# Kernel tuning notes

Measured on AMD Instinct MI355X. Metric: run time of the kernel, lower is better.

Reference implementation:

```python
import jax, jax.numpy as jnp
import numpy as np

HEADS = 12
DIM_HEAD = 64
SCALE = DIM_HEAD ** -0.5
LN_EPS = 1e-5


def _ternary(w):
    # BitNet-1.58-style ternary quantization with per-tensor absmean scale.
    s = jnp.mean(jnp.abs(w))
    return jnp.clip(jnp.round(w / (s + 1e-8)), -1.0, 1.0) * s


def _sparsify(x, sparsity):
    # Dynamic activation sparsity: zero the lowest-|x| `sparsity` fraction per token.
    thr = jnp.quantile(jnp.abs(x), sparsity, axis=-1, keepdims=True)
    return jnp.where(jnp.abs(x) >= thr, x, 0.0)


def setup_inputs() -> dict:
    key = jax.random.key(0)
    ks = jax.random.split(key, 4)
    b, n, dim = 16, 1024, 768
    inner = HEADS * DIM_HEAD
    return {
        "x": jax.random.normal(ks[0], (b, n, dim), dtype=jnp.float32),
        "gamma": jnp.ones((dim,), jnp.float32),
        "beta": jnp.zeros((dim,), jnp.float32),
        "w_qkv": jax.random.normal(ks[1], (3 * inner, dim), jnp.float32) * 0.02,
        "w_out": jax.random.normal(ks[2], (dim, inner), jnp.float32) * 0.02,
        "b_out": jnp.zeros((dim,), jnp.float32),
        "sparsity": jnp.float32(0.5),
    }


def reference(x, gamma, beta, w_qkv, w_out, b_out, sparsity):
    b, n, dim = x.shape
    # LayerNorm
    mu = jnp.mean(x, axis=-1, keepdims=True)
    var = jnp.mean((x - mu) ** 2, axis=-1, keepdims=True)
    xn = (x - mu) * jax.lax.rsqrt(var + LN_EPS) * gamma + beta
    # Sparse-ternary QKV projection (bias=False)
    qkv = jnp.einsum("bnd,ed->bne", _sparsify(xn, sparsity), _ternary(w_qkv))
    q, k, v = jnp.split(qkv, 3, axis=-1)
    def heads(t):  # b n (h d) -> b h n d
        return t.reshape(b, n, HEADS, DIM_HEAD).transpose(0, 2, 1, 3)
    q, k, v = heads(q), heads(k), heads(v)
    dots = jnp.einsum("bhid,bhjd->bhij", q, k) * SCALE
    attn = jax.nn.softmax(dots, axis=-1)
    out = jnp.einsum("bhij,bhjd->bhid", attn, v)
    out = out.transpose(0, 2, 1, 3).reshape(b, n, HEADS * DIM_HEAD)
    # Sparse-ternary output projection (with bias)
    out = jnp.einsum("bne,de->bnd", _sparsify(out, sparsity), _ternary(w_out)) + b_out
    return out
```

## Files before the change

kernel.cpp:

```cpp
#include <hip/hip_runtime.h>
#include <math.h>

#define TOKENS 16384
#define DIM    768
#define EDIM   2304
#define NHEADS 12
#define DHEAD  64
#define NQKVW  (EDIM*DIM)
#define NOUTW  (DIM*DIM)
#define LN_EPS 1e-5f

typedef __bf16 bf16x8 __attribute__((ext_vector_type(8)));
typedef float f32x4 __attribute__((ext_vector_type(4)));
typedef unsigned short u16x8 __attribute__((ext_vector_type(8)));
typedef unsigned short u16x4 __attribute__((ext_vector_type(4)));

__device__ __forceinline__ float wsum(float v){
#pragma unroll
  for(int m=1;m<64;m<<=1) v += __shfl_xor(v,m);
  return v;
}
__device__ __forceinline__ int wsumi(int v){
#pragma unroll
  for(int m=1;m<64;m<<=1) v += __shfl_xor(v,m);
  return v;
}
__device__ __forceinline__ unsigned wminu(unsigned v){
#pragma unroll
  for(int m=1;m<64;m<<=1){ unsigned o = __shfl_xor(v,m); v = (o<v)?o:v; }
  return v;
}

__device__ __forceinline__ unsigned short bf_rne(float x){
  unsigned u = __float_as_uint(x);
  unsigned r = (u + 0x7FFFu + ((u>>16)&1u)) >> 16;
  return (unsigned short)r;
}
__device__ __forceinline__ void split_bf(float x, unsigned short& h, unsigned short& l){
  h = bf_rne(x);
  float hf = __uint_as_float(((unsigned)h)<<16);
  l = bf_rne(x - hf);
}

__global__ __launch_bounds__(256) void absmean_kernel(
    const float* __restrict__ w1, int n1,
    const float* __restrict__ w2, int n2,
    double* __restrict__ sums){
  int stride = gridDim.x*blockDim.x;
  int i0 = blockIdx.x*blockDim.x + threadIdx.x;
  float s1=0.f, s2=0.f;
  for(int i=i0;i<n1;i+=stride) s1 += fabsf(w1[i]);
  for(int i=i0;i<n2;i+=stride) s2 += fabsf(w2[i]);
  double d1=(double)s1, d2=(double)s2;
#pragma unroll
  for(int m=1;m<64;m<<=1){ d1 += __shfl_xor(d1,m); d2 += __shfl_xor(d2,m); }
  __shared__ double l1[4], l2[4];
  int wv = threadIdx.x>>6;
  if((threadIdx.x&63)==0){ l1[wv]=d1; l2[wv]=d2; }
  __syncthreads();
  if(threadIdx.x==0){
    atomicAdd(&sums[0], l1[0]+l1[1]+l1[2]+l1[3]);
    atomicAdd(&sums[1], l2[0]+l2[1]+l2[2]+l2[3]);
  }
}

__global__ __launch_bounds__(256) void ternarize_kernel(
    const float* __restrict__ w, int n,
    const double* __restrict__ sums, int idx,
    unsigned short* __restrict__ o, float* __restrict__ scalef){
  float s  = (float)(sums[idx]/(double)n);
  float sd = s + 1e-8f;
  int i = blockIdx.x*blockDim.x + threadIdx.x;
  if(i<n){
    float t = rintf(w[i]/sd);
    t = fminf(fmaxf(t,-1.f),1.f);
    o[i] = bf_rne(t);
  }
  if(blockIdx.x==0 && threadIdx.x==0) scalef[idx] = s;
}

template<bool DO_LN>
__global__ __launch_bounds__(256) void ln_sparsify_kernel(
    const float* __restrict__ in,
    const float* __restrict__ gamma,
    const float* __restrict__ beta,
    const float* __restrict__ qp,
    unsigned short* __restrict__ oh,
    unsigned short* __restrict__ ol){
  int token = blockIdx.x*4 + (threadIdx.x>>6);
  int lane  = threadIdx.x & 63;
  const float* row = in + (size_t)token*DIM;
  float v[12];
#pragma unroll
  for(int g=0; g<3; ++g){
    float4 t = *(const float4*)(row + g*256 + lane*4);
    v[g*4+0]=t.x; v[g*4+1]=t.y; v[g*4+2]=t.z; v[g*4+3]=t.w;
  }
  float xn[12];
  if (DO_LN){
    float s=0.f;
#pragma unroll
    for(int i=0;i<12;i++) s += v[i];
    s = wsum(s);
    float mu = s*(1.f/768.f);
    float ss=0.f;
#pragma unroll
    for(int i=0;i<12;i++){ float d=v[i]-mu; ss += d*d; }
    ss = wsum(ss);
    float inv = 1.f/sqrtf(ss*(1.f/768.f) + LN_EPS);
#pragma unroll
    for(int g=0; g<3; ++g){
      float4 gm = *(const float4*)(gamma + g*256 + lane*4);
      float4 bt = *(const float4*)(beta  + g*256 + lane*4);
      xn[g*4+0] = (v[g*4+0]-mu)*inv*gm.x + bt.x;
      xn[g*4+1] = (v[g*4+1]-mu)*inv*gm.y + bt.y;
      xn[g*4+2] = (v[g*4+2]-mu)*inv*gm.z + bt.z;
      xn[g*4+3] = (v[g*4+3]-mu)*inv*gm.w + bt.w;
    }
  } else {
#pragma unroll
    for(int i=0;i<12;i++) xn[i]=v[i];
  }
  unsigned a[12];
#pragma unroll
  for(int i=0;i<12;i++) a[i] = __float_as_uint(fabsf(xn[i]));
  float q = *qp;
  float pos = q*767.f;
  int lo = (int)floorf(pos);
  lo = lo<0 ? 0 : (lo>767 ? 767 : lo);
  float frac = pos-(float)lo;
  unsigned prefix=0;
  int r = lo;
#pragma unroll 1
  for(int bit=30; bit>=0; --bit){
    unsigned cand = prefix | (1u<<bit);
    int c=0;
#pragma unroll
    for(int i=0;i<12;i++) c += (a[i]>=prefix && a[i]<cand) ? 1 : 0;
    c = wsumi(c);
    if(r>=c){ r-=c; prefix=cand; }
  }
  float f1 = __uint_as_float(prefix);
  float thr;
  if (frac>0.f && lo<767){
    int cle=0;
#pragma unroll
    for(int i=0;i<12;i++) cle += (a[i]<=prefix)?1:0;
    cle = wsumi(cle);
    unsigned mn=0xFFFFFFFFu;
#pragma unroll
    for(int i=0;i<12;i++){ if(a[i]>prefix && a[i]<mn) mn=a[i]; }
    mn = wminu(mn);
    float f2 = (cle>=lo+2) ? f1 : __uint_as_float(mn);
    thr = (frac>=0.5f) ? f2-(f2-f1)*(1.f-frac) : f1+(f2-f1)*frac;
  } else thr=f1;
  size_t obase = (size_t)token*DIM;
#pragma unroll
  for(int g=0; g<3; ++g){
    u16x4 hv, lv;
#pragma unroll
    for(int e=0;e<4;e++){
      float val = (fabsf(xn[g*4+e])>=thr) ? xn[g*4+e] : 0.f;
      unsigned short hh, ll;
      split_bf(val, hh, ll);
      hv[e]=hh; lv[e]=ll;
    }
    *(u16x4*)(oh + obase + g*256 + lane*4) = hv;
    *(u16x4*)(ol + obase + g*256 + lane*4) = lv;
  }
}

#define LDSW(row,c16) ((((row)*8 + ((c16) ^ ((row)&7))))*16)

template<int MODE>
__global__ __launch_bounds__(256) void gemm_sp_kernel(
    const unsigned short* __restrict__ ah, const unsigned short* __restrict__ al,
    const unsigned short* __restrict__ wt, const float* __restrict__ scalef,
    const float* __restrict__ bias,
    unsigned short* __restrict__ qh, unsigned short* __restrict__ ql,
    unsigned short* __restrict__ kh, unsigned short* __restrict__ kl,
    unsigned short* __restrict__ vth, unsigned short* __restrict__ vtl,
    float* __restrict__ outp){
  __shared__ __align__(16) char lds[49152];
  const int bm = blockIdx.y*128;
  const int bn = blockIdx.x*128;
  const int tid = threadIdx.x, w = tid>>6, l = tid&63, lq = l&15, g = l>>4;
  const int wm = (w>>1)*64, wn = (w&1)*64;

  const f32x4 zero4 = {0.f,0.f,0.f,0.f};
  f32x4 acc[4][4];
#pragma unroll
  for(int mt=0;mt<4;mt++)
#pragma unroll
    for(int nt=0;nt<4;nt++) acc[mt][nt]=zero4;

#pragma unroll 1
  for(int k0=0; k0<768; k0+=64){
    __syncthreads();
#pragma unroll
    for(int grp=0; grp<2; grp++){
      u16x8 tmp[6];
#pragma unroll
      for(int c=0;c<6;c++){
        int cc = grp*6 + c;
        int t = cc>>2;
        int slot = (cc&3)*256 + tid;
        int row = slot>>3, c8 = slot&7;
        int gc = ((c8 ^ (row&7)))<<3;
        const unsigned short* gp =
           (t==0) ? ah + (size_t)(bm+row)*768 + k0 + gc :
           (t==1) ? al + (size_t)(bm+row)*768 + k0 + gc :
                    wt + (size_t)(bn+row)*768 + k0 + gc;
        tmp[c] = *(const u16x8*)gp;
      }
#pragma unroll
      for(int c=0;c<6;c++){
        int cc = grp*6 + c;
        int t = cc>>2;
        int slot = (cc&3)*256 + tid;
        *(u16x8*)(lds + t*16384 + slot*16) = tmp[c];
      }
    }
    __syncthreads();
#pragma unroll
    for(int kc=0;kc<2;kc++){
      bf16x8 bfr[4];
#pragma unroll
      for(int nt=0;nt<4;nt++)
        bfr[nt] = *(const bf16x8*)(lds + 32768 + LDSW(wn+16*nt+lq, kc*4+g));
#pragma unroll
      for(int mt=0;mt<4;mt++){
        bf16x8 ahf = *(const bf16x8*)(lds +          LDSW(wm+16*mt+lq, kc*4+g));
        bf16x8 alf = *(const bf16x8*)(lds + 16384 +  LDSW(wm+16*mt+lq, kc*4+g));
#pragma unroll
        for(int nt=0;nt<4;nt++){
          acc[mt][nt] = __builtin_amdgcn_mfma_f32_16x16x32_bf16(ahf, bfr[nt], acc[mt][nt], 0,0,0);
          acc[mt][nt] = __builtin_amdgcn_mfma_f32_16x16x32_bf16(alf, bfr[nt], acc[mt][nt], 0,0,0);
        }
      }
    }
  }
  __syncthreads();

  if (MODE == 1){
    float s2 = scalef[1];
#pragma unroll
    for(int mt=0;mt<4;mt++)
#pragma unroll
      for(int nt=0;nt<4;nt++){
        int n = bn + wn + 16*nt + lq;
        float bs = bias[n];
#pragma unroll
        for(int r=0;r<4;r++){
          int m = bm + wm + 16*mt + 4*g + r;
          outp[(size_t)m*768 + n] = acc[mt][nt][r]*s2 + bs;
        }
      }
    return;
  }

  float s1 = scalef[0];
  if (bn < 1536){
    const bool isQ = bn < 768;
    const float sc = isQ ? s1*0.125f : s1;
    unsigned short* dh = isQ ? qh : kh;
    unsigned short* dl = isQ ? ql : kl;
    const int cb = isQ ? bn : bn-768;
    unsigned short* Th = (unsigned short*)lds;
    unsigned short* Tl = Th + 64*136;
#pragma unroll
    for(int p=0;p<2;p++){
      if(p) __syncthreads();
      if ((w>>1)==p){
#pragma unroll
        for(int mt=0;mt<4;mt++)
#pragma unroll
          for(int nt=0;nt<4;nt++)
#pragma unroll
            for(int r=0;r<4;r++){
              int mloc = 16*mt + 4*g + r;
              int c = wn + 16*nt + lq;
              unsigned short hh,ll;
              split_bf(acc[mt][nt][r]*sc, hh, ll);
              Th[mloc*136 + c] = hh;
              Tl[mloc*136 + c] = ll;
            }
      }
      __syncthreads();
      int mrow = tid>>2;
      int m = p*64 + mrow;
#pragma unroll
      for(int i=0;i<4;i++){
        int c8 = (tid&3)*4 + i;
        u16x8 hv = *(const u16x8*)(Th + mrow*136 + c8*8);
        u16x8 lv = *(const u16x8*)(Tl + mrow*136 + c8*8);
        size_t off = (size_t)(bm+m)*768 + cb + c8*8;
        *(u16x8*)(dh + off) = hv;
        *(u16x8*)(dl + off) = lv;
      }
    }
  } else {
    const int b  = bm >> 10;
    const int t0 = bm & 1023;
#pragma unroll
    for(int mt=0;mt<4;mt++)
#pragma unroll
      for(int nt=0;nt<4;nt++){
        int n = bn - 1536 + wn + 16*nt + lq;
        int hh_ = n>>6, d = n&63;
        u16x4 hv, lv;
#pragma unroll
        for(int r=0;r<4;r++){
          unsigned short h_, l_;
          split_bf(acc[mt][nt][r]*s1, h_, l_);
          hv[r]=h_; lv[r]=l_;
        }
        size_t off = ((size_t)(b*NHEADS + hh_)*64 + d)*1024 + t0 + wm + 16*mt + 4*g;
        *(u16x4*)(vth + off) = hv;
        *(u16x4*)(vtl + off) = lv;
      }
  }
}

__global__ __launch_bounds__(256) void attn_mfma_kernel(
    const unsigned short* __restrict__ qh, const unsigned short* __restrict__ ql,
    const unsigned short* __restrict__ kh, const unsigned short* __restrict__ kl,
    const unsigned short* __restrict__ vh, const unsigned short* __restrict__ vl,
    float* __restrict__ ao){
  __shared__ __align__(16) char lds[32768];
  const int qb=blockIdx.x, h=blockIdx.y, b=blockIdx.z;
  const int tid=threadIdx.x, w=tid>>6, l=tid&63, lq=l&15, g=l>>4;

  const int qtok = b*1024 + qb*64 + w*16 + lq;
  bf16x8 qhf[2], qlf[2];
  {
    const size_t qo = (size_t)qtok*768 + h*64 + g*8;
    qhf[0] = *(const bf16x8*)(qh + qo);
    qhf[1] = *(const bf16x8*)(qh + qo + 32);
    qlf[0] = *(const bf16x8*)(ql + qo);
    qlf[1] = *(const bf16x8*)(ql + qo + 32);
  }
  const f32x4 zero4 = {0.f,0.f,0.f,0.f};
  f32x4 o[4];
#pragma unroll
  for(int mt=0;mt<4;mt++) o[mt]=zero4;
  float ms = -INFINITY, ls = 0.f;

  for(int kt=0; kt<16; ++kt){
    __syncthreads();
#pragma unroll
    for(int m=0;m<4;m++){
      const unsigned short* src = (m==0)?kh:(m==1)?kl:(m==2)?vh:vl;
#pragma unroll
      for(int half=0; half<2; half++){
        int a = half*256 + tid;
        int row = a>>3;
        int c16 = (a&7)^(row&7);
        size_t goff = (m<2)
          ? ((size_t)(b*1024 + kt*64 + row)*768 + h*64 + c16*8)
          : (((size_t)(b*NHEADS + h)*64 + row)*1024 + kt*64 + c16*8);
        u16x8 v = *(const u16x8*)(src + goff);
        *(u16x8*)(lds + m*8192 + a*16) = v;
      }
    }
    __syncthreads();
    f32x4 s[4];
#pragma unroll
    for(int mt=0;mt<4;mt++) s[mt]=zero4;
#pragma unroll
    for(int kc=0;kc<2;kc++){
#pragma unroll
      for(int mt=0;mt<4;mt++){
        bf16x8 ka = *(const bf16x8*)(lds + 0*8192 + LDSW(16*mt+lq, 4*kc+g));
        bf16x8 kb = *(const bf16x8*)(lds + 1*8192 + LDSW(16*mt+lq, 4*kc+g));
        s[mt] = __builtin_amdgcn_mfma_f32_16x16x32_bf16(ka, qhf[kc], s[mt], 0,0,0);
        s[mt] = __builtin_amdgcn_mfma_f32_16x16x32_bf16(ka, qlf[kc], s[mt], 0,0,0);
        s[mt] = __builtin_amdgcn_mfma_f32_16x16x32_bf16(kb, qhf[kc], s[mt], 0,0,0);
      }
    }
    float pm = -INFINITY;
#pragma unroll
    for(int mt=0;mt<4;mt++)
#pragma unroll
      for(int r=0;r<4;r++) pm = fmaxf(pm, s[mt][r]);
    pm = fmaxf(pm, __shfl_xor(pm,16));
    pm = fmaxf(pm, __shfl_xor(pm,32));
    float mn = fmaxf(ms, pm);
    float alpha = __expf(ms - mn);
    float p[4][4];
    float rs = 0.f;
#pragma unroll
    for(int mt=0;mt<4;mt++)
#pragma unroll
      for(int r=0;r<4;r++){ float pv=__expf(s[mt][r]-mn); p[mt][r]=pv; rs+=pv; }
    rs += __shfl_xor(rs,16);
    rs += __shfl_xor(rs,32);
    ls = ls*alpha + rs; ms = mn;
#pragma unroll
    for(int mt=0;mt<4;mt++) o[mt] *= alpha;
    bf16x8 pfh[2], pfl[2];
#pragma unroll
    for(int c=0;c<2;c++){
      u16x8 hu, lu;
#pragma unroll
      for(int j=0;j<8;j++){
        int srcLane = lq + (((g&1)*2 + (j>>2))<<4);
        float va = __shfl(p[2*c  ][j&3], srcLane);
        float vb = __shfl(p[2*c+1][j&3], srcLane);
        float v = (g>>1) ? vb : va;
        unsigned short hh, ll;
        split_bf(v, hh, ll);
        hu[j]=hh; lu[j]=ll;
      }
      pfh[c] = __builtin_bit_cast(bf16x8, hu);
      pfl[c] = __builtin_bit_cast(bf16x8, lu);
    }
#pragma unroll
    for(int kc=0;kc<2;kc++){
#pragma unroll
      for(int mt=0;mt<4;mt++){
        bf16x8 va_ = *(const bf16x8*)(lds + 2*8192 + LDSW(16*mt+lq, 4*kc+g));
        bf16x8 vb_ = *(const bf16x8*)(lds + 3*8192 + LDSW(16*mt+lq, 4*kc+g));
        o[mt] = __builtin_amdgcn_mfma_f32_16x16x32_bf16(va_, pfh[kc], o[mt], 0,0,0);
        o[mt] = __builtin_amdgcn_mfma_f32_16x16x32_bf16(va_, pfl[kc], o[mt], 0,0,0);
        o[mt] = __builtin_amdgcn_mfma_f32_16x16x32_bf16(vb_, pfh[kc], o[mt], 0,0,0);
        o[mt] = __builtin_amdgcn_mfma_f32_16x16x32_bf16(vb_, pfl[kc], o[mt], 0,0,0);
      }
    }
  }
  float inv = 1.f/ls;
  float* orow = ao + (size_t)qtok*DIM + h*64;
#pragma unroll
  for(int mt=0;mt<4;mt++){
    f32x4 st = o[mt]*inv;
    *(f32x4*)(orow + mt*16 + g*4) = st;
  }
}

extern "C" void kernel_launch(void* const* d_in, const int* in_sizes, int n_in,
                              void* d_out, int out_size, void* d_ws, size_t ws_size,
                              hipStream_t stream){
  const float* x      = (const float*)d_in[0];
  const float* gamma  = (const float*)d_in[1];
  const float* beta   = (const float*)d_in[2];
  const float* w_qkv  = (const float*)d_in[3];
  const float* w_out  = (const float*)d_in[4];
  const float* b_out  = (const float*)d_in[5];
  const float* spars  = (const float*)d_in[6];
  float* out = (float*)d_out;

  double* sums  = (double*)d_ws;
  float* scalef = (float*)((char*)d_ws + 16);
  unsigned short* wt_qkv = (unsigned short*)((char*)d_ws + 64);
  unsigned short* wt_out = wt_qkv + NQKVW;
  unsigned short* ahb = wt_out + NOUTW;
  unsigned short* alb = ahb + (size_t)TOKENS*DIM;
  unsigned short* qh  = alb + (size_t)TOKENS*DIM;
  unsigned short* ql  = qh  + (size_t)TOKENS*DIM;
  unsigned short* kh  = ql  + (size_t)TOKENS*DIM;
  unsigned short* kl  = kh  + (size_t)TOKENS*DIM;
  unsigned short* vth = kl  + (size_t)TOKENS*DIM;
  unsigned short* vtl = vth + (size_t)TOKENS*DIM;
  float* ao = (float*)(vtl + (size_t)TOKENS*DIM);

  hipMemsetAsync(d_ws, 0, 16, stream);
  absmean_kernel<<<1024,256,0,stream>>>(w_qkv, NQKVW, w_out, NOUTW, sums);
  ternarize_kernel<<<(NQKVW+255)/256,256,0,stream>>>(w_qkv, NQKVW, sums, 0, wt_qkv, scalef);
  ternarize_kernel<<<(NOUTW+255)/256,256,0,stream>>>(w_out, NOUTW, sums, 1, wt_out, scalef);
  ln_sparsify_kernel<true><<<TOKENS/4,256,0,stream>>>(x, gamma, beta, spars, ahb, alb);
  gemm_sp_kernel<0><<<dim3(EDIM/128, TOKENS/128),256,0,stream>>>(
      ahb, alb, wt_qkv, scalef, nullptr, qh, ql, kh, kl, vth, vtl, nullptr);
  attn_mfma_kernel<<<dim3(16,NHEADS,16),256,0,stream>>>(qh, ql, kh, kl, vth, vtl, ao);
  ln_sparsify_kernel<false><<<TOKENS/4,256,0,stream>>>(ao, nullptr, nullptr, spars, ahb, alb);
  gemm_sp_kernel<1><<<dim3(DIM/128, TOKENS/128),256,0,stream>>>(
      ahb, alb, wt_out, scalef, b_out, nullptr, nullptr, nullptr, nullptr, nullptr, nullptr, out);
}
```

Measured before the change: 840.6 us.

## Add XCD-aware block remapping, larger attention blocks, and native bf16 conversions

The GEMM kernels now take a 1D grid and remap block ids so that consecutive tiles land on the same XCD, which should improve L2 reuse of A and weight tiles. The attention kernel moves to 512 threads covering 128 queries per block, also with XCD-grouped (batch, head) assignment, so each K/V tile loaded into LDS serves twice as many queries. Its LDS fill becomes one 16-byte load per tensor per thread. bf16 rounding now uses native __bf16 casts instead of manual bit arithmetic. The larger block may lower occupancy, and the remap assumes the hardware dispatches blocks round-robin across 8 XCDs.

```diff
diff --git a/kernel.cpp b/kernel.cpp
--- a/kernel.cpp
+++ b/kernel.cpp
@@ -31,15 +31,16 @@
   return v;
 }
 
+__device__ __forceinline__ void split_bf(float x, unsigned short& h, unsigned short& l){
+  __bf16 hb = (__bf16)x;
+  float hf = (float)hb;
+  __bf16 lb = (__bf16)(x - hf);
+  h = __builtin_bit_cast(unsigned short, hb);
+  l = __builtin_bit_cast(unsigned short, lb);
+}
 __device__ __forceinline__ unsigned short bf_rne(float x){
-  unsigned u = __float_as_uint(x);
-  unsigned r = (u + 0x7FFFu + ((u>>16)&1u)) >> 16;
-  return (unsigned short)r;
-}
-__device__ __forceinline__ void split_bf(float x, unsigned short& h, unsigned short& l){
-  h = bf_rne(x);
-  float hf = __uint_as_float(((unsigned)h)<<16);
-  l = bf_rne(x - hf);
+  __bf16 hb = (__bf16)x;
+  return __builtin_bit_cast(unsigned short, hb);
 }
 
 __global__ __launch_bounds__(256) void absmean_kernel(
@@ -182,8 +183,15 @@
     unsigned short* __restrict__ vth, unsigned short* __restrict__ vtl,
     float* __restrict__ outp){
   __shared__ __align__(16) char lds[49152];
-  const int bm = blockIdx.y*128;
-  const int bn = blockIdx.x*128;
+  const int NB = (MODE==0) ? 18 : 6;
+  const int nwg = NB*128;
+  int flat = blockIdx.x;
+  {
+    int xcd = flat & 7, idx = flat >> 3;
+    flat = xcd*(nwg>>3) + idx;
+  }
+  const int bm = (flat / NB)*128;
+  const int bn = (flat % NB)*128;
   const int tid = threadIdx.x, w = tid>>6, l = tid&63, lq = l&15, g = l>>4;
   const int wm = (w>>1)*64, wn = (w&1)*64;
 
@@ -322,16 +330,20 @@
   }
 }
 
-__global__ __launch_bounds__(256) void attn_mfma_kernel(
+__global__ __launch_bounds__(512) void attn_mfma_kernel(
     const unsigned short* __restrict__ qh, const unsigned short* __restrict__ ql,
     const unsigned short* __restrict__ kh, const unsigned short* __restrict__ kl,
     const unsigned short* __restrict__ vh, const unsigned short* __restrict__ vl,
     float* __restrict__ ao){
   __shared__ __align__(16) char lds[32768];
-  const int qb=blockIdx.x, h=blockIdx.y, b=blockIdx.z;
+  int flat = blockIdx.x;
+  int xcd = flat & 7, r_ = flat >> 3;
+  int pair = xcd*24 + (r_ >> 3);
+  int qb = r_ & 7;
+  int h = pair % NHEADS, b = pair / NHEADS;
   const int tid=threadIdx.x, w=tid>>6, l=tid&63, lq=l&15, g=l>>4;
 
-  const int qtok = b*1024 + qb*64 + w*16 + lq;
+  const int qtok = b*1024 + qb*128 + w*16 + lq;
   bf16x8 qhf[2], qlf[2];
   {
     const size_t qo = (size_t)qtok*768 + h*64 + g*8;
@@ -346,22 +358,23 @@
   for(int mt=0;mt<4;mt++) o[mt]=zero4;
   float ms = -INFINITY, ls = 0.f;
 
+#pragma unroll 1
   for(int kt=0; kt<16; ++kt){
     __syncthreads();
-#pragma unroll
-    for(int m=0;m<4;m++){
-      const unsigned short* src = (m==0)?kh:(m==1)?kl:(m==2)?vh:vl;
-#pragma unroll
-      for(int half=0; half<2; half++){
-        int a = half*256 + tid;
-        int row = a>>3;
-        int c16 = (a&7)^(row&7);
-        size_t goff = (m<2)
-          ? ((size_t)(b*1024 + kt*64 + row)*768 + h*64 + c16*8)
-          : (((size_t)(b*NHEADS + h)*64 + row)*1024 + kt*64 + c16*8);
-        u16x8 v = *(const u16x8*)(src + goff);
-        *(u16x8*)(lds + m*8192 + a*16) = v;
-      }
+    {
+      int a = tid;
+      int row = a>>3;
+      int c16 = (a&7)^(row&7);
+      size_t koff = (size_t)(b*1024 + kt*64 + row)*768 + h*64 + c16*8;
+      size_t voff = ((size_t)(b*NHEADS + h)*64 + row)*1024 + kt*64 + c16*8;
+      u16x8 v0 = *(const u16x8*)(kh + koff);
+      u16x8 v1 = *(const u16x8*)(kl + koff);
+      u16x8 v2 = *(const u16x8*)(vh + voff);
+      u16x8 v3 = *(const u16x8*)(vl + voff);
+      *(u16x8*)(lds + 0*8192 + a*16) = v0;
+      *(u16x8*)(lds + 1*8192 + a*16) = v1;
+      *(u16x8*)(lds + 2*8192 + a*16) = v2;
+      *(u16x8*)(lds + 3*8192 + a*16) = v3;
     }
     __syncthreads();
     f32x4 s[4];
@@ -468,10 +481,10 @@
   ternarize_kernel<<<(NQKVW+255)/256,256,0,stream>>>(w_qkv, NQKVW, sums, 0, wt_qkv, scalef);
   ternarize_kernel<<<(NOUTW+255)/256,256,0,stream>>>(w_out, NOUTW, sums, 1, wt_out, scalef);
   ln_sparsify_kernel<true><<<TOKENS/4,256,0,stream>>>(x, gamma, beta, spars, ahb, alb);
-  gemm_sp_kernel<0><<<dim3(EDIM/128, TOKENS/128),256,0,stream>>>(
+  gemm_sp_kernel<0><<<2304,256,0,stream>>>(
       ahb, alb, wt_qkv, scalef, nullptr, qh, ql, kh, kl, vth, vtl, nullptr);
-  attn_mfma_kernel<<<dim3(16,NHEADS,16),256,0,stream>>>(qh, ql, kh, kl, vth, vtl, ao);
+  attn_mfma_kernel<<<1536,512,0,stream>>>(qh, ql, kh, kl, vth, vtl, ao);
   ln_sparsify_kernel<false><<<TOKENS/4,256,0,stream>>>(ao, nullptr, nullptr, spars, ahb, alb);
-  gemm_sp_kernel<1><<<dim3(DIM/128, TOKENS/128),256,0,stream>>>(
+  gemm_sp_kernel<1><<<768,256,0,stream>>>(
       ahb, alb, wt_out, scalef, b_out, nullptr, nullptr, nullptr, nullptr, nullptr, nullptr, out);
 }
```

Result: faster. 743.5 us (-11.6%).
